# Kernel tuning notes

Hardware: AMD Instinct MI355X
Metric: run time of the kernel (lower is better)

Reference implementation:

```python
import jax, jax.numpy as jnp
import numpy as np

KL_W = 0.001
DENSITY_W = 0.1
SIZING_W = 0.05
BIG = 1e6


def _pairwise_sqdist(x, y):
    # x: [B,N,3], y: [B,M,3] -> [B,N,M] squared euclidean distances
    x2 = jnp.sum(x * x, axis=-1)  # [B,N]
    y2 = jnp.sum(y * y, axis=-1)  # [B,M]
    xy = jnp.einsum('bnd,bmd->bnm', x, y)
    return x2[:, :, None] + y2[:, None, :] - 2.0 * xy


def setup_inputs() -> dict:
    key = jax.random.key(0)
    ks = jax.random.split(key, 6)
    B, N, D, L = 4, 4096, 3, 512
    return {
        'pred_pos': jax.random.normal(ks[0], (B, N, D), dtype=jnp.float32),
        'pred_sizing': jax.random.uniform(ks[1], (B, N), dtype=jnp.float32),
        'target_pos': jax.random.normal(ks[2], (B, N, D), dtype=jnp.float32),
        'target_sizing': jax.random.uniform(ks[3], (B, N), dtype=jnp.float32),
        'mu': jax.random.normal(ks[4], (B, L), dtype=jnp.float32),
        'logvar': jax.random.normal(ks[5], (B, L), dtype=jnp.float32),
    }


def reference(pred_pos, pred_sizing, target_pos, target_sizing, mu, logvar):
    # Chamfer distance (bidirectional)
    dist = _pairwise_sqdist(pred_pos, target_pos)  # [B,N,M]
    d_p2t = jnp.min(dist, axis=2).mean(axis=1)     # [B]
    d_t2p = jnp.min(dist, axis=1).mean(axis=1)     # [B]
    cd = jnp.mean(d_p2t + d_t2p)

    # KL divergence term
    kl = -0.5 * jnp.mean(1.0 + logvar - mu * mu - jnp.exp(logvar))

    # Density uniformity: std (ddof=1, torch default) of nearest-neighbor sq-dist
    N = pred_pos.shape[1]
    d_self = _pairwise_sqdist(pred_pos, pred_pos)
    d_self = d_self + jnp.eye(N, dtype=d_self.dtype)[None] * BIG
    nn_d = jnp.min(d_self, axis=2)                 # [B,N]
    density = jnp.mean(jnp.std(nn_d, axis=1, ddof=1))

    # Sizing MSE
    sizing = jnp.mean((pred_sizing - target_sizing) ** 2)

    total = cd + KL_W * kl + DENSITY_W * density + SIZING_W * sizing
    return total
```

## Files before the change

kernel.cpp:

```cpp
#include <hip/hip_runtime.h>
#include <cfloat>
#include <cmath>

#define NB     4
#define NPTS   4096
#define NLAT   512
#define RPTS   16
#define CJ     64
#define NJC    (NPTS / CJ)

__global__ __launch_bounds__(256) void k_min_dist(
    const float* __restrict__ pred_pos,
    const float* __restrict__ targ_pos,
    float* __restrict__ part_mins )
{
    __shared__ float4 lds[CJ];

    const int tid  = threadIdx.x;
    const int jc   = blockIdx.x & (NJC - 1);
    const int b    = (blockIdx.x >> 6) & 3;
    const int mode = blockIdx.x >> 8;

    const float* pts = (mode == 1) ? targ_pos : pred_pos;
    const float* oth = (mode == 0) ? targ_pos : pred_pos;

    const int j0 = jc * CJ;
    if (tid < CJ) {
        const float* ob = oth + ((size_t)b * NPTS + j0) * 3;
        const float ox = ob[3 * tid], oy = ob[3 * tid + 1], oz = ob[3 * tid + 2];
        const float o2 = fmaf(oz, oz, fmaf(oy, oy, ox * ox));
        lds[tid] = make_float4(-2.f * ox, -2.f * oy, -2.f * oz, o2);
    }

    const float* pb = pts + (size_t)b * NPTS * 3;
    float px[RPTS], py[RPTS], pz[RPTS], p2[RPTS], acc[RPTS];
    #pragma unroll
    for (int k = 0; k < RPTS; ++k) {
        const int i = tid + (k << 8);
        px[k] = pb[3 * i];
        py[k] = pb[3 * i + 1];
        pz[k] = pb[3 * i + 2];
        p2[k] = fmaf(pz[k], pz[k], fmaf(py[k], py[k], px[k] * px[k]));
        acc[k] = FLT_MAX;
    }
    __syncthreads();

    if (mode != 2) {
        #pragma unroll 2
        for (int j = 0; j < CJ; ++j) {
            const float4 o = lds[j];
            #pragma unroll
            for (int k = 0; k < RPTS; ++k) {
                float t = fmaf(o.x, px[k], o.w);
                t = fmaf(o.y, py[k], t);
                t = fmaf(o.z, pz[k], t);
                acc[k] = fminf(acc[k], t);
            }
        }
    } else {
        #pragma unroll 2
        for (int j = 0; j < CJ; ++j) {
            const float4 o = lds[j];
            const int rel = (j0 + j) - tid;
            #pragma unroll
            for (int k = 0; k < RPTS; ++k) {
                float t = fmaf(o.x, px[k], o.w);
                t = fmaf(o.y, py[k], t);
                t = fmaf(o.z, pz[k], t);
                t = (rel == (k << 8)) ? FLT_MAX : t;
                acc[k] = fminf(acc[k], t);
            }
        }
    }

    float* mbase = part_mins + (((size_t)mode * NB + b) * NJC + jc) * NPTS;
    #pragma unroll
    for (int k = 0; k < RPTS; ++k)
        mbase[tid + (k << 8)] = acc[k] + p2[k];
}

__device__ __forceinline__ float block_sum(float v, float* red)
{
    #pragma unroll
    for (int o = 32; o >= 1; o >>= 1) v += __shfl_xor(v, o);
    const int w = threadIdx.x >> 6;
    __syncthreads();
    if ((threadIdx.x & 63) == 0) red[w] = v;
    __syncthreads();
    return red[0] + red[1] + red[2] + red[3];
}

__global__ __launch_bounds__(256) void k_fold(
    const float* __restrict__ part_mins,
    float* __restrict__ sums ,
    float* __restrict__ sumsqs )
{
    __shared__ float red[4];
    const int blk  = blockIdx.x;
    const int q    = blk & 3;
    const int b    = (blk >> 2) & 3;
    const int mode = blk >> 4;
    const float* base = part_mins + ((size_t)mode * NB + b) * NJC * NPTS;

    const int i0 = q * 1024 + threadIdx.x;
    float m[4] = {FLT_MAX, FLT_MAX, FLT_MAX, FLT_MAX};
    for (int jc = 0; jc < NJC; ++jc) {
        const float* row = base + (size_t)jc * NPTS + i0;
        #pragma unroll
        for (int t = 0; t < 4; ++t)
            m[t] = fminf(m[t], row[t * 256]);
    }
    float s = 0.f, s2 = 0.f;
    #pragma unroll
    for (int t = 0; t < 4; ++t) { s += m[t]; s2 = fmaf(m[t], m[t], s2); }

    s  = block_sum(s,  red);
    s2 = block_sum(s2, red);
    if (threadIdx.x == 0) { sums[blk] = s; sumsqs[blk] = s2; }
}

__global__ __launch_bounds__(256) void k_finalize(
    const float* __restrict__ pred_sizing,
    const float* __restrict__ targ_sizing,
    const float* __restrict__ mu,
    const float* __restrict__ logvar,
    const float* __restrict__ sums,
    const float* __restrict__ sumsqs,
    float* __restrict__ out)
{
    __shared__ float red[4];
    const int tid = threadIdx.x;

    float kls = 0.f;
    for (int i = tid; i < NB * NLAT; i += 256) {
        const float lv = logvar[i], m = mu[i];
        kls += 1.f + lv - m * m - expf(lv);
    }
    float szs = 0.f;
    for (int i = tid; i < NB * NPTS; i += 256) {
        const float d = pred_sizing[i] - targ_sizing[i];
        szs += d * d;
    }
    kls = block_sum(kls, red);
    szs = block_sum(szs, red);

    if (tid == 0) {
        float cd_sum = 0.f, dens_sum = 0.f;
        for (int b = 0; b < NB; ++b) {
            float s01 = 0.f, sS = 0.f, sS2 = 0.f;
            for (int q = 0; q < 4; ++q) {
                s01 += sums[b * 4 + q] + sums[16 + b * 4 + q];
                sS  += sums[32 + b * 4 + q];
                sS2 += sumsqs[32 + b * 4 + q];
            }
            cd_sum += s01 / (float)NPTS;
            const float var = (sS2 - sS * sS / (float)NPTS) / (float)(NPTS - 1);
            dens_sum += sqrtf(fmaxf(var, 0.f));
        }
        const float cd     = cd_sum / (float)NB;
        const float dens   = dens_sum / (float)NB;
        const float kl     = -0.5f * kls / (float)(NB * NLAT);
        const float sizing = szs / (float)(NB * NPTS);
        out[0] = cd + 0.001f * kl + 0.1f * dens + 0.05f * sizing;
    }
}

extern "C" void kernel_launch(void* const* d_in, const int* in_sizes, int n_in,
                              void* d_out, int out_size, void* d_ws, size_t ws_size,
                              hipStream_t stream)
{
    const float* pred_pos    = (const float*)d_in[0];
    const float* pred_sizing = (const float*)d_in[1];
    const float* targ_pos    = (const float*)d_in[2];
    const float* targ_sizing = (const float*)d_in[3];
    const float* mu          = (const float*)d_in[4];
    const float* logvar      = (const float*)d_in[5];

    float* part_mins = (float*)d_ws;
    float* sums      = part_mins + (size_t)3 * NB * NJC * NPTS;
    float* sumsqs    = sums + 48;

    k_min_dist<<<dim3(3 * NB * NJC), dim3(256), 0, stream>>>(
        pred_pos, targ_pos, part_mins);
    k_fold<<<dim3(48), dim3(256), 0, stream>>>(part_mins, sums, sumsqs);
    k_finalize<<<dim3(1), dim3(256), 0, stream>>>(
        pred_sizing, targ_sizing, mu, logvar, sums, sumsqs, (float*)d_out);
}
```

Measured before the change: 46.62 us.

## Precompute transformed points, read them directly, hoist self-mask, widen fold grid

Adds a prep kernel that writes the -2x,-2y,-2z,|p|^2 float4 form of every point to workspace. The main kernel then reads the other-point chunk straight from global memory (uniform loads) instead of staging it through LDS, which drops the __syncthreads. The self-distance mode no longer masks inside the inner loop; it computes the diagonal-affected point separately and patches it in afterwards. The fold kernel goes from 48 to 192 blocks for more parallelism, at the cost of one more kernel launch and larger partial-sum buffers.

```diff
diff --git a/kernel.cpp b/kernel.cpp
--- a/kernel.cpp
+++ b/kernel.cpp
@@ -9,74 +9,107 @@
 #define CJ     64
 #define NJC    (NPTS / CJ)
 
+__global__ __launch_bounds__(256) void k_prep(
+    const float* __restrict__ pred_pos, const float* __restrict__ targ_pos,
+    float4* __restrict__ predT, float4* __restrict__ targT)
+{
+    const int i = blockIdx.x * 256 + threadIdx.x;
+    {
+        const float x = pred_pos[3*i], y = pred_pos[3*i+1], z = pred_pos[3*i+2];
+        predT[i] = make_float4(-2.f*x, -2.f*y, -2.f*z, fmaf(z,z,fmaf(y,y,x*x)));
+    }
+    {
+        const float x = targ_pos[3*i], y = targ_pos[3*i+1], z = targ_pos[3*i+2];
+        targT[i] = make_float4(-2.f*x, -2.f*y, -2.f*z, fmaf(z,z,fmaf(y,y,x*x)));
+    }
+}
+
 __global__ __launch_bounds__(256) void k_min_dist(
     const float* __restrict__ pred_pos,
     const float* __restrict__ targ_pos,
+    const float4* __restrict__ predT,
+    const float4* __restrict__ targT,
     float* __restrict__ part_mins )
 {
-    __shared__ float4 lds[CJ];
-
     const int tid  = threadIdx.x;
     const int jc   = blockIdx.x & (NJC - 1);
     const int b    = (blockIdx.x >> 6) & 3;
     const int mode = blockIdx.x >> 8;
 
-    const float* pts = (mode == 1) ? targ_pos : pred_pos;
-    const float* oth = (mode == 0) ? targ_pos : pred_pos;
-
-    const int j0 = jc * CJ;
-    if (tid < CJ) {
-        const float* ob = oth + ((size_t)b * NPTS + j0) * 3;
-        const float ox = ob[3 * tid], oy = ob[3 * tid + 1], oz = ob[3 * tid + 2];
-        const float o2 = fmaf(oz, oz, fmaf(oy, oy, ox * ox));
-        lds[tid] = make_float4(-2.f * ox, -2.f * oy, -2.f * oz, o2);
-    }
-
-    const float* pb = pts + (size_t)b * NPTS * 3;
-    float px[RPTS], py[RPTS], pz[RPTS], p2[RPTS], acc[RPTS];
+    const float*  pb  = ((mode == 1) ? targ_pos : pred_pos) + (size_t)b * NPTS * 3;
+    const float4* ob4 = ((mode == 0) ? targT : predT) + (size_t)b * NPTS + jc * CJ;
+
+    float px[RPTS], py[RPTS], pz[RPTS], acc[RPTS];
     #pragma unroll
     for (int k = 0; k < RPTS; ++k) {
         const int i = tid + (k << 8);
-        px[k] = pb[3 * i];
-        py[k] = pb[3 * i + 1];
-        pz[k] = pb[3 * i + 2];
-        p2[k] = fmaf(pz[k], pz[k], fmaf(py[k], py[k], px[k] * px[k]));
+        px[k] = pb[3*i]; py[k] = pb[3*i+1]; pz[k] = pb[3*i+2];
         acc[k] = FLT_MAX;
     }
-    __syncthreads();
 
     if (mode != 2) {
         #pragma unroll 2
-        for (int j = 0; j < CJ; ++j) {
-            const float4 o = lds[j];
+        for (int j = 0; j < CJ; j += 2) {
+            const float4 o1 = ob4[j];
+            const float4 o2 = ob4[j + 1];
             #pragma unroll
             for (int k = 0; k < RPTS; ++k) {
-                float t = fmaf(o.x, px[k], o.w);
-                t = fmaf(o.y, py[k], t);
-                t = fmaf(o.z, pz[k], t);
-                acc[k] = fminf(acc[k], t);
+                float t1 = fmaf(o1.x, px[k], o1.w);
+                t1 = fmaf(o1.y, py[k], t1);
+                t1 = fmaf(o1.z, pz[k], t1);
+                float t2 = fmaf(o2.x, px[k], o2.w);
+                t2 = fmaf(o2.y, py[k], t2);
+                t2 = fmaf(o2.z, pz[k], t2);
+                acc[k] = fminf(acc[k], fminf(t1, t2));
             }
         }
     } else {
+        const int  kself = jc >> 2;
+        const bool aff   = (tid >> 6) == (jc & 3);
+        const int  jself = tid & 63;
+        float sx = 0.f, sy = 0.f, sz = 0.f;
+        #pragma unroll
+        for (int k = 0; k < RPTS; ++k) {
+            sx = (k == kself) ? px[k] : sx;
+            sy = (k == kself) ? py[k] : sy;
+            sz = (k == kself) ? pz[k] : sz;
+        }
+        float accf = FLT_MAX;
         #pragma unroll 2
-        for (int j = 0; j < CJ; ++j) {
-            const float4 o = lds[j];
-            const int rel = (j0 + j) - tid;
+        for (int j = 0; j < CJ; j += 2) {
+            const float4 o1 = ob4[j];
+            const float4 o2 = ob4[j + 1];
             #pragma unroll
             for (int k = 0; k < RPTS; ++k) {
-                float t = fmaf(o.x, px[k], o.w);
-                t = fmaf(o.y, py[k], t);
-                t = fmaf(o.z, pz[k], t);
-                t = (rel == (k << 8)) ? FLT_MAX : t;
-                acc[k] = fminf(acc[k], t);
+                float t1 = fmaf(o1.x, px[k], o1.w);
+                t1 = fmaf(o1.y, py[k], t1);
+                t1 = fmaf(o1.z, pz[k], t1);
+                float t2 = fmaf(o2.x, px[k], o2.w);
+                t2 = fmaf(o2.y, py[k], t2);
+                t2 = fmaf(o2.z, pz[k], t2);
+                acc[k] = fminf(acc[k], fminf(t1, t2));
             }
-        }
+            float f1 = fmaf(o1.x, sx, o1.w);
+            f1 = fmaf(o1.y, sy, f1);
+            f1 = fmaf(o1.z, sz, f1);
+            f1 = (j == jself) ? FLT_MAX : f1;
+            float f2 = fmaf(o2.x, sx, o2.w);
+            f2 = fmaf(o2.y, sy, f2);
+            f2 = fmaf(o2.z, sz, f2);
+            f2 = ((j + 1) == jself) ? FLT_MAX : f2;
+            accf = fminf(accf, fminf(f1, f2));
+        }
+        #pragma unroll
+        for (int k = 0; k < RPTS; ++k)
+            acc[k] = (aff && k == kself) ? accf : acc[k];
     }
 
     float* mbase = part_mins + (((size_t)mode * NB + b) * NJC + jc) * NPTS;
     #pragma unroll
-    for (int k = 0; k < RPTS; ++k)
-        mbase[tid + (k << 8)] = acc[k] + p2[k];
+    for (int k = 0; k < RPTS; ++k) {
+        const float p2 = fmaf(pz[k], pz[k], fmaf(py[k], py[k], px[k]*px[k]));
+        mbase[tid + (k << 8)] = acc[k] + p2;
+    }
 }
 
 __device__ __forceinline__ float block_sum(float v, float* red)
@@ -92,30 +125,21 @@
 
 __global__ __launch_bounds__(256) void k_fold(
     const float* __restrict__ part_mins,
-    float* __restrict__ sums ,
-    float* __restrict__ sumsqs )
+    float* __restrict__ sums , float* __restrict__ sumsqs )
 {
     __shared__ float red[4];
-    const int blk  = blockIdx.x;
-    const int q    = blk & 3;
-    const int b    = (blk >> 2) & 3;
-    const int mode = blk >> 4;
-    const float* base = part_mins + ((size_t)mode * NB + b) * NJC * NPTS;
-
-    const int i0 = q * 1024 + threadIdx.x;
-    float m[4] = {FLT_MAX, FLT_MAX, FLT_MAX, FLT_MAX};
-    for (int jc = 0; jc < NJC; ++jc) {
-        const float* row = base + (size_t)jc * NPTS + i0;
-        #pragma unroll
-        for (int t = 0; t < 4; ++t)
-            m[t] = fminf(m[t], row[t * 256]);
-    }
-    float s = 0.f, s2 = 0.f;
-    #pragma unroll
-    for (int t = 0; t < 4; ++t) { s += m[t]; s2 = fmaf(m[t], m[t], s2); }
-
-    s  = block_sum(s,  red);
-    s2 = block_sum(s2, red);
+    const int blk   = blockIdx.x;
+    const int slice = blk & 15;
+    const int b     = (blk >> 4) & 3;
+    const int mode  = blk >> 6;
+    const float* base = part_mins + ((size_t)mode * NB + b) * NJC * NPTS
+                        + slice * 256 + threadIdx.x;
+    float m = FLT_MAX;
+    #pragma unroll 8
+    for (int jc = 0; jc < NJC; ++jc)
+        m = fminf(m, base[(size_t)jc * NPTS]);
+    const float s  = block_sum(m, red);
+    const float s2 = block_sum(m * m, red);
     if (threadIdx.x == 0) { sums[blk] = s; sumsqs[blk] = s2; }
 }
 
@@ -137,6 +161,7 @@
         kls += 1.f + lv - m * m - expf(lv);
     }
     float szs = 0.f;
+    #pragma unroll 4
     for (int i = tid; i < NB * NPTS; i += 256) {
         const float d = pred_sizing[i] - targ_sizing[i];
         szs += d * d;
@@ -148,10 +173,10 @@
         float cd_sum = 0.f, dens_sum = 0.f;
         for (int b = 0; b < NB; ++b) {
             float s01 = 0.f, sS = 0.f, sS2 = 0.f;
-            for (int q = 0; q < 4; ++q) {
-                s01 += sums[b * 4 + q] + sums[16 + b * 4 + q];
-                sS  += sums[32 + b * 4 + q];
-                sS2 += sumsqs[32 + b * 4 + q];
+            for (int s = 0; s < 16; ++s) {
+                s01 += sums[b * 16 + s] + sums[64 + b * 16 + s];
+                sS  += sums[128 + b * 16 + s];
+                sS2 += sumsqs[128 + b * 16 + s];
             }
             cd_sum += s01 / (float)NPTS;
             const float var = (sS2 - sS * sS / (float)NPTS) / (float)(NPTS - 1);
@@ -176,13 +201,17 @@
     const float* mu          = (const float*)d_in[4];
     const float* logvar      = (const float*)d_in[5];
 
-    float* part_mins = (float*)d_ws;
-    float* sums      = part_mins + (size_t)3 * NB * NJC * NPTS;
-    float* sumsqs    = sums + 48;
-
+    float4* predT = (float4*)d_ws;
+    float4* targT = predT + (size_t)NB * NPTS;
+    float*  part_mins = (float*)(targT + (size_t)NB * NPTS);
+    float*  sums   = part_mins + (size_t)3 * NB * NJC * NPTS;
+    float*  sumsqs = sums + 192;
+
+    k_prep<<<dim3(NB * NPTS / 256), dim3(256), 0, stream>>>(
+        pred_pos, targ_pos, predT, targT);
     k_min_dist<<<dim3(3 * NB * NJC), dim3(256), 0, stream>>>(
-        pred_pos, targ_pos, part_mins);
-    k_fold<<<dim3(48), dim3(256), 0, stream>>>(part_mins, sums, sumsqs);
+        pred_pos, targ_pos, predT, targT, part_mins);
+    k_fold<<<dim3(192), dim3(256), 0, stream>>>(part_mins, sums, sumsqs);
     k_finalize<<<dim3(1), dim3(256), 0, stream>>>(
         pred_sizing, targ_sizing, mu, logvar, sums, sumsqs, (float*)d_out);
 }
```

New measurement: 58.37 us. +25.2%, slower.
